# Optimization experiments

Hardware: AMD Instinct MI355X
Metric: run time of the kernel (lower is better)

## Reference

```python
import jax, jax.numpy as jnp
import numpy as np

DIM = 1024
WIN = 7
HEADS = 16
HEAD_DIM = DIM // HEADS
NT = WIN * WIN  # tokens per window = 49


def _relative_position_index():
    coords = np.stack(np.meshgrid(np.arange(WIN), np.arange(WIN), indexing='ij'))  # [2,W,W]
    cf = coords.reshape(2, -1)  # [2, NT]
    rel = cf[:, :, None] - cf[:, None, :]  # [2, NT, NT]
    rel = rel.transpose(1, 2, 0).copy()
    rel[:, :, 0] += WIN - 1
    rel[:, :, 1] += WIN - 1
    rel[:, :, 0] *= 2 * WIN - 1
    return jnp.asarray(rel.sum(-1), dtype=jnp.int32)  # [NT, NT]

REL_IDX = _relative_position_index()


def setup_inputs() -> dict:
    key = jax.random.key(0)
    ks = jax.random.split(key, 7)
    bsz_windows = 2048
    num_windows = 64
    x = jax.random.normal(ks[0], (bsz_windows, NT, DIM), dtype=jnp.float32)
    attn_mask = jax.random.normal(ks[1], (num_windows, NT, NT), dtype=jnp.float32)
    s = 0.02
    qkv_w = jax.random.normal(ks[2], (3 * DIM, DIM), dtype=jnp.float32) * s
    qkv_b = jnp.zeros((3 * DIM,), dtype=jnp.float32)
    proj_w = jax.random.normal(ks[3], (DIM, DIM), dtype=jnp.float32) * s
    proj_b = jnp.zeros((DIM,), dtype=jnp.float32)
    bias_table = jax.random.normal(ks[4], ((2 * WIN - 1) ** 2, HEADS), dtype=jnp.float32) * s
    return {"x": x, "attn_mask": attn_mask, "qkv_w": qkv_w, "qkv_b": qkv_b,
            "proj_w": proj_w, "proj_b": proj_b, "bias_table": bias_table}


def reference(x, attn_mask, qkv_w, qkv_b, proj_w, proj_b, bias_table):
    bw, nt, c = x.shape
    scale = HEAD_DIM ** -0.5
    qkv = x @ qkv_w.T + qkv_b  # [bw, nt, 3*dim]
    qkv = qkv.reshape(bw, nt, 3, HEADS, HEAD_DIM).transpose(2, 0, 3, 1, 4)
    q, k, v = qkv[0], qkv[1], qkv[2]  # each [bw, h, nt, hd]
    attn = jnp.einsum('bhqd,bhkd->bhqk', q * scale, k)  # [bw, h, nt, nt]
    rel_bias = bias_table[REL_IDX.reshape(-1)].reshape(nt, nt, HEADS).transpose(2, 0, 1)
    attn = attn + rel_bias[None]
    nw = attn_mask.shape[0]
    attn = attn.reshape(bw // nw, nw, HEADS, nt, nt) + attn_mask[None, :, None]
    attn = attn.reshape(bw, HEADS, nt, nt)
    attn = jax.nn.softmax(attn, axis=-1)
    out = jnp.einsum('bhqk,bhkd->bhqd', attn, v)
    out = out.transpose(0, 2, 1, 3).reshape(bw, nt, c)
    return out @ proj_w.T + proj_b
```

## Files before the change

### kernel.cpp

```cpp
#include <hip/hip_runtime.h>
#include <hip/hip_bf16.h>
#include <cstdint>
#include <cstddef>

#define HEADS 16
#define HD 64
#define NT 49
#define NTOK 3136
#define MROWS 100352
#define KDIM 1024

typedef __attribute__((ext_vector_type(4))) float f32x4;
typedef __attribute__((ext_vector_type(8))) short bf16x8;
typedef __attribute__((ext_vector_type(4))) unsigned short u16x4;

__device__ __forceinline__ unsigned short f2b(float f) {
  __hip_bfloat16 h = __float2bfloat16(f);
  return *reinterpret_cast<unsigned short*>(&h);
}
__device__ __forceinline__ float b2f(unsigned short u) {
  union { unsigned int i; float f; } c; c.i = ((unsigned int)u) << 16; return c.f;
}

__device__ __forceinline__ void gload16(const unsigned short* g, void* l) {
  __builtin_amdgcn_global_load_lds(
      (const __attribute__((address_space(1))) void*)g,
      (__attribute__((address_space(3))) void*)l, 16, 0, 0);
}

__device__ __forceinline__ void bar() {
  asm volatile("" ::: "memory");
  __builtin_amdgcn_s_barrier();
  asm volatile("" ::: "memory");
}

__global__ void cvt_f32_bf16(const float* __restrict__ s,
                             unsigned short* __restrict__ d, long n4) {
  long stride = (long)gridDim.x * blockDim.x;
  for (long i = blockIdx.x * (long)blockDim.x + threadIdx.x; i < n4; i += stride) {
    f32x4 v = reinterpret_cast<const f32x4*>(s)[i];
    u16x4 o;
    o.x = f2b(v.x); o.y = f2b(v.y); o.z = f2b(v.z); o.w = f2b(v.w);
    reinterpret_cast<u16x4*>(d)[i] = o;
  }
}

__global__ void build_bm(const float* __restrict__ mask,
                         const float* __restrict__ bias_table,
                         float* __restrict__ bm) {
  const int wm = blockIdx.x >> 4, h = blockIdx.x & 15;
  const float* mrow = mask + (size_t)wm * (NT * NT);
  float* dst = bm + ((size_t)wm * HEADS + h) * (NT * 64);
  for (int idx = threadIdx.x; idx < NT * 64; idx += 256) {
    const int a = idx >> 6, b = idx & 63;
    float v = -1e30f;
    if (b < NT) {
      const int ia = a / 7, ja = a - ia * 7;
      const int ib = b / 7, jb = b - ib * 7;
      v = mrow[a * NT + b] +
          bias_table[((ia - ib + 6) * 13 + (ja - jb + 6)) * HEADS + h];
    }
    dst[idx] = v;
  }
}

template<int EPI>
__global__ __launch_bounds__(512, 4)
void gemm_bt(const unsigned short* __restrict__ A,
             const unsigned short* __restrict__ B,
             const float* __restrict__ bias,
             void* __restrict__ Cout,
             const int nTilesN) {
  __shared__ __align__(16) unsigned short lds[2 * 12288];

  const int nwg = gridDim.x;
  const int bid = blockIdx.x;
  const int cpx = nwg >> 3;
  const int swz = (bid & 7) * cpx + (bid >> 3);
  const int mt = swz / nTilesN;
  const int nt = swz - mt * nTilesN;
  const long mBase = (long)mt * 256;
  const int nBase = nt * 128;

  const int tid = threadIdx.x;
  const int lane = tid & 63;
  const int wid = tid >> 6;
  const int wr = wid >> 1;
  const int wc = wid & 1;
  const int lr = lane & 15;
  const int kg = lane >> 4;

  const int srow = tid >> 2;
  const int c8 = (((tid & 3) ^ ((tid >> 3) & 3)) << 3);
  const unsigned short* aSrc0 = A + (size_t)(mBase + srow) * KDIM + c8;
  const unsigned short* aSrc1 = aSrc0 + (size_t)128 * KDIM;
  const unsigned short* bSrc  = B + (size_t)(nBase + srow) * KDIM + c8;
  char* ldsB = (char*)lds;

  f32x4 acc[4][4] = {};

  int aOff[4], bOff[4];
#pragma unroll
  for (int m = 0; m < 4; ++m) {
    const int row = wr * 64 + m * 16 + lr;
    aOff[m] = row * 32 + ((kg ^ ((row >> 1) & 3)) << 3);
  }
#pragma unroll
  for (int n = 0; n < 4; ++n) {
    const int row = wc * 64 + n * 16 + lr;
    bOff[n] = row * 32 + ((kg ^ ((row >> 1) & 3)) << 3);
  }

#define STAGE(buf, kt) do {                               \
    char* dst = ldsB + (buf) * 24576 + tid * 16;          \
    gload16(aSrc0 + (kt) * 32, dst);                      \
    gload16(aSrc1 + (kt) * 32, dst + 8192);               \
    gload16(bSrc  + (kt) * 32, dst + 16384);              \
  } while (0)

  STAGE(0, 0);
  STAGE(1, 1);
  asm volatile("s_waitcnt vmcnt(3)" ::: "memory");
  __builtin_amdgcn_sched_barrier(0);
  bar();

  for (int kt = 0; kt < KDIM / 32; ++kt) {
    const int cb = kt & 1;
    const unsigned short* As = lds + cb * 12288;
    const unsigned short* Bs = As + 8192;

    bf16x8 af[4], bfv[4];
#pragma unroll
    for (int m = 0; m < 4; ++m)
      af[m] = *reinterpret_cast<const bf16x8*>(As + aOff[m]);
#pragma unroll
    for (int n = 0; n < 4; ++n)
      bfv[n] = *reinterpret_cast<const bf16x8*>(Bs + bOff[n]);

    __builtin_amdgcn_s_setprio(1);
#pragma unroll
    for (int m = 0; m < 4; ++m)
#pragma unroll
      for (int n = 0; n < 4; ++n)
        acc[m][n] = __builtin_amdgcn_mfma_f32_16x16x32_bf16(
            af[m], bfv[n], acc[m][n], 0, 0, 0);
    __builtin_amdgcn_s_setprio(0);
    bar();

    if (kt < KDIM / 32 - 2) {
      STAGE(cb, kt + 2);
      asm volatile("s_waitcnt vmcnt(3)" ::: "memory");
      __builtin_amdgcn_sched_barrier(0);
      bar();
    } else if (kt == KDIM / 32 - 2) {
      asm volatile("s_waitcnt vmcnt(0)" ::: "memory");
      __builtin_amdgcn_sched_barrier(0);
      bar();
    }
  }
#undef STAGE

  if (EPI == 0) {
    unsigned short* qkvbuf = (unsigned short*)Cout;
#pragma unroll
    for (int m = 0; m < 4; ++m) {
      const int row0 = wr * 64 + m * 16 + kg * 4;
#pragma unroll
      for (int n = 0; n < 4; ++n) {
        const int col = nBase + wc * 64 + n * 16 + lr;
        const int which = col >> 10;
        const int head = (col >> 6) & 15;
        const int d = col & 63;
        const float bv = bias[col];
#pragma unroll
        for (int r = 0; r < 4; ++r) {
          const int gm = (int)mBase + row0 + r;
          const int w = gm / NT;
          const int t = gm - w * NT;
          float v = acc[m][n][r] + bv;
          if (which == 0) v *= 0.125f;
          qkvbuf[(((size_t)w * 3 + which) * HEADS + head) * NTOK + t * HD + d] =
              f2b(v);
        }
      }
    }
  } else {
    float* out = (float*)Cout;
#pragma unroll
    for (int m = 0; m < 4; ++m) {
      const int row0 = wr * 64 + m * 16 + kg * 4;
#pragma unroll
      for (int n = 0; n < 4; ++n) {
        const int col = nBase + wc * 64 + n * 16 + lr;
        const float bv = bias[col];
#pragma unroll
        for (int r = 0; r < 4; ++r) {
          const int gm = (int)mBase + row0 + r;
          out[(size_t)gm * KDIM + col] = acc[m][n][r] + bv;
        }
      }
    }
  }
}

#define PSTR 72
#define VTSTR 72

__global__ __launch_bounds__(256, 8)
void attn_mfma(const unsigned short* __restrict__ qkv,
               const float* __restrict__ bm,
               unsigned short* __restrict__ aout) {
  const int blk = blockIdx.x;
  const int w = blk >> 4;
  const int h = blk & 15;
  const int tid = threadIdx.x;
  const int lane = tid & 63;
  const int wv = tid >> 6;
  const int lr = lane & 15;
  const int kg = lane >> 4;

  __shared__ __align__(16) unsigned short Plds[64 * PSTR];
  __shared__ __align__(16) unsigned short VldsT[64 * VTSTR];

  const unsigned short* qp = qkv + (((size_t)w * 3 + 0) * HEADS + h) * NTOK;
  const unsigned short* kp = qp + (size_t)HEADS * NTOK;
  const unsigned short* vp = qp + (size_t)2 * HEADS * NTOK;
  const float* bmrow = bm + (((size_t)(w & 63) * HEADS + h) * (NT * 64));

  const int a0 = wv * 16 + kg * 4;
  f32x4 acc[4];
#pragma unroll
  for (int r = 0; r < 4; ++r) {
    const int a = a0 + r;
    const int ar = (a > 48) ? 48 : a;
#pragma unroll
    for (int n = 0; n < 4; ++n)
      acc[n][r] = bmrow[ar * 64 + n * 16 + lr];
  }

#pragma unroll
  for (int i = 0; i < 4; ++i) {
    const int idx = i * 256 + tid;
    if (idx < 784) {
      const int t = idx >> 4, c4 = (idx & 15) * 4;
      u16x4 vv = *reinterpret_cast<const u16x4*>(vp + t * HD + c4);
      const int ts = t >> 3, t7 = t & 7;
#pragma unroll
      for (int ii = 0; ii < 4; ++ii) {
        const int d = c4 + ii;
        VldsT[d * VTSTR + (((ts ^ (d & 7)) << 3) + t7)] =
            ((const unsigned short*)&vv)[ii];
      }
    }
  }
#pragma unroll
  for (int i = 0; i < 4; ++i) {
    const int idx = i * 256 + tid;
    if (idx < 960) {
      const int d = idx / 15, t = 49 + idx - d * 15;
      VldsT[d * VTSTR + ((((t >> 3) ^ (d & 7)) << 3) + (t & 7))] = 0;
    }
  }
  __syncthreads();

  int qrow = wv * 16 + lr; if (qrow > 48) qrow = 48;
#pragma unroll
  for (int ks = 0; ks < 2; ++ks) {
    bf16x8 af = *reinterpret_cast<const bf16x8*>(qp + qrow * HD + ks * 32 + kg * 8);
#pragma unroll
    for (int n = 0; n < 4; ++n) {
      int row = n * 16 + lr; if (row > 48) row = 48;
      bf16x8 bfr = *reinterpret_cast<const bf16x8*>(kp + row * HD + ks * 32 + kg * 8);
      acc[n] = __builtin_amdgcn_mfma_f32_16x16x32_bf16(af, bfr, acc[n], 0, 0, 0);
    }
  }

#pragma unroll
  for (int r = 0; r < 4; ++r) {
    float mx = fmaxf(fmaxf(acc[0][r], acc[1][r]),
                     fmaxf(acc[2][r], acc[3][r]));
    mx = fmaxf(mx, __shfl_xor(mx, 1));
    mx = fmaxf(mx, __shfl_xor(mx, 2));
    mx = fmaxf(mx, __shfl_xor(mx, 4));
    mx = fmaxf(mx, __shfl_xor(mx, 8));
    float s = 0.f;
#pragma unroll
    for (int n = 0; n < 4; ++n) {
      const float e = __expf(acc[n][r] - mx);
      acc[n][r] = e;
      s += e;
    }
    s += __shfl_xor(s, 1);
    s += __shfl_xor(s, 2);
    s += __shfl_xor(s, 4);
    s += __shfl_xor(s, 8);
    const float si = 1.0f / s;
#pragma unroll
    for (int n = 0; n < 4; ++n) acc[n][r] *= si;
  }

#pragma unroll
  for (int n = 0; n < 4; ++n)
#pragma unroll
    for (int r = 0; r < 4; ++r)
      Plds[(a0 + r) * PSTR + n * 16 + lr] = f2b(acc[n][r]);

  f32x4 acc2[4] = {};
  const int prow = wv * 16 + lr;
#pragma unroll
  for (int ks = 0; ks < 2; ++ks) {
    bf16x8 pf = *reinterpret_cast<const bf16x8*>(
        &Plds[prow * PSTR + ks * 32 + kg * 8]);
#pragma unroll
    for (int n = 0; n < 4; ++n) {
      const int d = n * 16 + lr;
      bf16x8 vf = *reinterpret_cast<const bf16x8*>(
          &VldsT[d * VTSTR + ((((ks * 4 + kg) ^ (d & 7)) << 3))]);
      acc2[n] = __builtin_amdgcn_mfma_f32_16x16x32_bf16(pf, vf, acc2[n], 0, 0, 0);
    }
  }

#pragma unroll
  for (int r = 0; r < 4; ++r) {
    const int a = a0 + r;
    if (a >= NT) continue;
#pragma unroll
    for (int n = 0; n < 4; ++n) {
      const int d = n * 16 + lr;
      aout[((size_t)(w * NT + a)) * KDIM + h * HD + d] = f2b(acc2[n][r]);
    }
  }
}

extern "C" void kernel_launch(void* const* d_in, const int* in_sizes, int n_in,
                              void* d_out, int out_size, void* d_ws, size_t ws_size,
                              hipStream_t stream) {
  const float* x          = (const float*)d_in[0];
  const float* attn_mask  = (const float*)d_in[1];
  const float* qkv_w      = (const float*)d_in[2];
  const float* qkv_b      = (const float*)d_in[3];
  const float* proj_w     = (const float*)d_in[4];
  const float* proj_b     = (const float*)d_in[5];
  const float* bias_table = (const float*)d_in[6];
  float* out = (float*)d_out;

  char* ws = (char*)d_ws;
  const size_t xbf_bytes = (size_t)MROWS * KDIM * 2;
  const size_t qkv_bytes = (size_t)2048 * 3 * HEADS * NTOK * 2;
  unsigned short* xbf      = (unsigned short*)ws;
  unsigned short* qkvw_bf  = (unsigned short*)(ws + xbf_bytes);
  unsigned short* projw_bf = qkvw_bf + 3072 * 1024;
  unsigned short* qkvbuf   = (unsigned short*)(ws + xbf_bytes + 8388608);
  float* bm                = (float*)(ws + xbf_bytes + 8388608 + qkv_bytes);
  unsigned short* aout     = xbf;

  build_bm<<<64 * HEADS, 256, 0, stream>>>(attn_mask, bias_table, bm);

  cvt_f32_bf16<<<8192, 256, 0, stream>>>(x, xbf, (long)MROWS * KDIM / 4);
  cvt_f32_bf16<<<3072, 256, 0, stream>>>(qkv_w, qkvw_bf, (long)3072 * 1024 / 4);
  cvt_f32_bf16<<<1024, 256, 0, stream>>>(proj_w, projw_bf, (long)1024 * 1024 / 4);

  gemm_bt<0><<<392 * 24, 512, 0, stream>>>(xbf, qkvw_bf, qkv_b, (void*)qkvbuf, 24);

  attn_mfma<<<2048 * HEADS, 256, 0, stream>>>(qkvbuf, bm, aout);

  gemm_bt<1><<<392 * 8, 512, 0, stream>>>(aout, projw_bf, proj_b, (void*)out, 8);
}
```

Measured before the change: 1.360 ms.

## Fuse fp32-to-bf16 conversion of x into QKV GEMM A-tile loading

Removes the standalone conversion kernel for x. The QKV GEMM now loads fp32 A rows into registers, converts them to bf16 and writes them into the swizzled LDS tile, while B keeps using async global-to-LDS loads. This avoids a full fp32 read plus bf16 write/read pass over the large activation. In exchange, every N-tile block rereads A in fp32 (double bytes), and the A loads become register-staged instead of direct-to-LDS, adding register pressure and waits.

Measured after the change: 1.419 ms. +4.4%, slower.

```diff
diff --git a/kernel.cpp b/kernel.cpp
--- a/kernel.cpp
+++ b/kernel.cpp
@@ -32,6 +32,14 @@
   asm volatile("" ::: "memory");
   __builtin_amdgcn_s_barrier();
   asm volatile("" ::: "memory");
+}
+
+struct alignas(16) u16x8s { u16x4 a, b; };
+__device__ __forceinline__ void write16(void* dst, f32x4 a, f32x4 b) {
+  u16x8s v;
+  v.a.x = f2b(a.x); v.a.y = f2b(a.y); v.a.z = f2b(a.z); v.a.w = f2b(a.w);
+  v.b.x = f2b(b.x); v.b.y = f2b(b.y); v.b.z = f2b(b.z); v.b.w = f2b(b.w);
+  *reinterpret_cast<u16x8s*>(dst) = v;
 }
 
 __global__ void cvt_f32_bf16(const float* __restrict__ s,
@@ -66,7 +74,7 @@
 
 template<int EPI>
 __global__ __launch_bounds__(512, 4)
-void gemm_bt(const unsigned short* __restrict__ A,
+void gemm_bt(const void* __restrict__ Ap,
              const unsigned short* __restrict__ B,
              const float* __restrict__ bias,
              void* __restrict__ Cout,
@@ -92,9 +100,7 @@
 
   const int srow = tid >> 2;
   const int c8 = (((tid & 3) ^ ((tid >> 3) & 3)) << 3);
-  const unsigned short* aSrc0 = A + (size_t)(mBase + srow) * KDIM + c8;
-  const unsigned short* aSrc1 = aSrc0 + (size_t)128 * KDIM;
-  const unsigned short* bSrc  = B + (size_t)(nBase + srow) * KDIM + c8;
+  const unsigned short* bSrc = B + (size_t)(nBase + srow) * KDIM + c8;
   char* ldsB = (char*)lds;
 
   f32x4 acc[4][4] = {};
@@ -110,6 +116,83 @@
     const int row = wc * 64 + n * 16 + lr;
     bOff[n] = row * 32 + ((kg ^ ((row >> 1) & 3)) << 3);
   }
+
+  if (EPI == 0) {
+    const float* aF0 = (const float*)Ap + (size_t)(mBase + srow) * KDIM + c8;
+    const float* aF1 = aF0 + (size_t)128 * KDIM;
+
+    f32x4 r0a, r0b, r1a, r1b;
+
+    r0a = *reinterpret_cast<const f32x4*>(aF0 + 0);
+    r0b = *reinterpret_cast<const f32x4*>(aF0 + 4);
+    r1a = *reinterpret_cast<const f32x4*>(aF1 + 0);
+    r1b = *reinterpret_cast<const f32x4*>(aF1 + 4);
+    gload16(bSrc + 0, ldsB + 16384 + tid * 16);
+    write16(ldsB + tid * 16, r0a, r0b);
+    write16(ldsB + 8192 + tid * 16, r1a, r1b);
+    r0a = *reinterpret_cast<const f32x4*>(aF0 + 32);
+    r0b = *reinterpret_cast<const f32x4*>(aF0 + 36);
+    r1a = *reinterpret_cast<const f32x4*>(aF1 + 32);
+    r1b = *reinterpret_cast<const f32x4*>(aF1 + 36);
+    gload16(bSrc + 32, ldsB + 24576 + 16384 + tid * 16);
+    asm volatile("s_waitcnt vmcnt(5)" ::: "memory");
+    asm volatile("s_waitcnt lgkmcnt(0)" ::: "memory");
+    __builtin_amdgcn_sched_barrier(0);
+    bar();
+
+    for (int kt = 0; kt < 32; ++kt) {
+      const int cb = kt & 1;
+      const unsigned short* As = lds + cb * 12288;
+      const unsigned short* Bs = As + 8192;
+
+      bf16x8 af[4], bfv[4];
+#pragma unroll
+      for (int m = 0; m < 4; ++m)
+        af[m] = *reinterpret_cast<const bf16x8*>(As + aOff[m]);
+#pragma unroll
+      for (int n = 0; n < 4; ++n)
+        bfv[n] = *reinterpret_cast<const bf16x8*>(Bs + bOff[n]);
+
+      if (kt < 31) {
+        char* dA = ldsB + (cb ^ 1) * 24576 + tid * 16;
+        write16(dA, r0a, r0b);
+        write16(dA + 8192, r1a, r1b);
+        if (kt < 30) {
+          const int off = (kt + 2) * 32;
+          r0a = *reinterpret_cast<const f32x4*>(aF0 + off);
+          r0b = *reinterpret_cast<const f32x4*>(aF0 + off + 4);
+          r1a = *reinterpret_cast<const f32x4*>(aF1 + off);
+          r1b = *reinterpret_cast<const f32x4*>(aF1 + off + 4);
+        }
+      }
+
+      __builtin_amdgcn_s_setprio(1);
+#pragma unroll
+      for (int m = 0; m < 4; ++m)
+#pragma unroll
+        for (int n = 0; n < 4; ++n)
+          acc[m][n] = __builtin_amdgcn_mfma_f32_16x16x32_bf16(
+              af[m], bfv[n], acc[m][n], 0, 0, 0);
+      __builtin_amdgcn_s_setprio(0);
+      asm volatile("s_waitcnt lgkmcnt(0)" ::: "memory");
+      bar();
+
+      if (kt < 30) {
+        gload16(bSrc + (kt + 2) * 32,
+                ldsB + cb * 24576 + 16384 + tid * 16);
+        asm volatile("s_waitcnt vmcnt(5)" ::: "memory");
+        __builtin_amdgcn_sched_barrier(0);
+        bar();
+      } else if (kt == 30) {
+        asm volatile("s_waitcnt vmcnt(0)" ::: "memory");
+        __builtin_amdgcn_sched_barrier(0);
+        bar();
+      }
+    }
+  } else {
+    const unsigned short* aSrc0 =
+        (const unsigned short*)Ap + (size_t)(mBase + srow) * KDIM + c8;
+    const unsigned short* aSrc1 = aSrc0 + (size_t)128 * KDIM;
 
 #define STAGE(buf, kt) do {                               \
     char* dst = ldsB + (buf) * 24576 + tid * 16;          \
@@ -118,47 +201,48 @@
     gload16(bSrc  + (kt) * 32, dst + 16384);              \
   } while (0)
 
-  STAGE(0, 0);
-  STAGE(1, 1);
-  asm volatile("s_waitcnt vmcnt(3)" ::: "memory");
-  __builtin_amdgcn_sched_barrier(0);
-  bar();
-
-  for (int kt = 0; kt < KDIM / 32; ++kt) {
-    const int cb = kt & 1;
-    const unsigned short* As = lds + cb * 12288;
-    const unsigned short* Bs = As + 8192;
-
-    bf16x8 af[4], bfv[4];
-#pragma unroll
-    for (int m = 0; m < 4; ++m)
-      af[m] = *reinterpret_cast<const bf16x8*>(As + aOff[m]);
-#pragma unroll
-    for (int n = 0; n < 4; ++n)
-      bfv[n] = *reinterpret_cast<const bf16x8*>(Bs + bOff[n]);
-
-    __builtin_amdgcn_s_setprio(1);
-#pragma unroll
-    for (int m = 0; m < 4; ++m)
+    STAGE(0, 0);
+    STAGE(1, 1);
+    asm volatile("s_waitcnt vmcnt(3)" ::: "memory");
+    __builtin_amdgcn_sched_barrier(0);
+    bar();
+
+    for (int kt = 0; kt < 32; ++kt) {
+      const int cb = kt & 1;
+      const unsigned short* As = lds + cb * 12288;
+      const unsigned short* Bs = As + 8192;
+
+      bf16x8 af[4], bfv[4];
+#pragma unroll
+      for (int m = 0; m < 4; ++m)
+        af[m] = *reinterpret_cast<const bf16x8*>(As + aOff[m]);
 #pragma unroll
       for (int n = 0; n < 4; ++n)
-        acc[m][n] = __builtin_amdgcn_mfma_f32_16x16x32_bf16(
-            af[m], bfv[n], acc[m][n], 0, 0, 0);
-    __builtin_amdgcn_s_setprio(0);
-    bar();
-
-    if (kt < KDIM / 32 - 2) {
-      STAGE(cb, kt + 2);
-      asm volatile("s_waitcnt vmcnt(3)" ::: "memory");
-      __builtin_amdgcn_sched_barrier(0);
+        bfv[n] = *reinterpret_cast<const bf16x8*>(Bs + bOff[n]);
+
+      __builtin_amdgcn_s_setprio(1);
+#pragma unroll
+      for (int m = 0; m < 4; ++m)
+#pragma unroll
+        for (int n = 0; n < 4; ++n)
+          acc[m][n] = __builtin_amdgcn_mfma_f32_16x16x32_bf16(
+              af[m], bfv[n], acc[m][n], 0, 0, 0);
+      __builtin_amdgcn_s_setprio(0);
       bar();
-    } else if (kt == KDIM / 32 - 2) {
-      asm volatile("s_waitcnt vmcnt(0)" ::: "memory");
-      __builtin_amdgcn_sched_barrier(0);
-      bar();
-    }
-  }
+
+      if (kt < 30) {
+        STAGE(cb, kt + 2);
+        asm volatile("s_waitcnt vmcnt(3)" ::: "memory");
+        __builtin_amdgcn_sched_barrier(0);
+        bar();
+      } else if (kt == 30) {
+        asm volatile("s_waitcnt vmcnt(0)" ::: "memory");
+        __builtin_amdgcn_sched_barrier(0);
+        bar();
+      }
+    }
 #undef STAGE
+  }
 
   if (EPI == 0) {
     unsigned short* qkvbuf = (unsigned short*)Cout;
@@ -347,22 +431,22 @@
   char* ws = (char*)d_ws;
   const size_t xbf_bytes = (size_t)MROWS * KDIM * 2;
   const size_t qkv_bytes = (size_t)2048 * 3 * HEADS * NTOK * 2;
-  unsigned short* xbf      = (unsigned short*)ws;
   unsigned short* qkvw_bf  = (unsigned short*)(ws + xbf_bytes);
   unsigned short* projw_bf = qkvw_bf + 3072 * 1024;
   unsigned short* qkvbuf   = (unsigned short*)(ws + xbf_bytes + 8388608);
   float* bm                = (float*)(ws + xbf_bytes + 8388608 + qkv_bytes);
-  unsigned short* aout     = xbf;
+  unsigned short* aout     = (unsigned short*)ws;
 
   build_bm<<<64 * HEADS, 256, 0, stream>>>(attn_mask, bias_table, bm);
 
-  cvt_f32_bf16<<<8192, 256, 0, stream>>>(x, xbf, (long)MROWS * KDIM / 4);
   cvt_f32_bf16<<<3072, 256, 0, stream>>>(qkv_w, qkvw_bf, (long)3072 * 1024 / 4);
   cvt_f32_bf16<<<1024, 256, 0, stream>>>(proj_w, projw_bf, (long)1024 * 1024 / 4);
 
-  gemm_bt<0><<<392 * 24, 512, 0, stream>>>(xbf, qkvw_bf, qkv_b, (void*)qkvbuf, 24);
+  gemm_bt<0><<<392 * 24, 512, 0, stream>>>((const void*)x, qkvw_bf, qkv_b,
+                                           (void*)qkvbuf, 24);
 
   attn_mfma<<<2048 * HEADS, 256, 0, stream>>>(qkvbuf, bm, aout);
 
-  gemm_bt<1><<<392 * 8, 512, 0, stream>>>(aout, projw_bf, proj_b, (void*)out, 8);
-}
+  gemm_bt<1><<<392 * 8, 512, 0, stream>>>((const void*)aout, projw_bf, proj_b,
+                                          (void*)out, 8);
+}
```
